# Optimization experiments

Measured on AMD Instinct MI355X. Metric: run time of the kernel, lower is better.

The kernel has to match this reference:

```python
import jax, jax.numpy as jnp
import numpy as np

B = 65536
N_FEATURES = 96
N_TOKENS = 32      # ceil(96/3)
DEPTH = 6
N_Q3_LAYERS = 6    # stem + 4 residual + 1 reduce (3to1)
N_CLASSES = 10


def setup_inputs() -> dict:
    key = jax.random.key(0)
    k1, k2, k3 = jax.random.split(key, 3)
    x_ = jax.random.normal(k1, (B, N_FEATURES), dtype=jnp.float32)
    # packed per-layer, per-block StronglyEntanglingLayers weights: (n_layers, n_tokens, depth, 3, 3)
    thetas = 0.01 * jax.random.normal(k2, (N_Q3_LAYERS, N_TOKENS, DEPTH, 3, 3), dtype=jnp.float32)
    w_cls = jax.random.normal(k3, (N_CLASSES, N_TOKENS), dtype=jnp.float32) / np.sqrt(N_TOKENS)
    b_cls = jnp.zeros((N_CLASSES,), dtype=jnp.float32)
    return {"x_": x_, "thetas": thetas, "w_cls": w_cls, "b_cls": b_cls}


def _rot(phi, theta, omega):
    """PennyLane Rot(phi,theta,omega) matrix, elementwise over leading dims -> (...,2,2) complex64."""
    ct = jnp.cos(0.5 * theta)
    st = jnp.sin(0.5 * theta)
    m00 = jnp.exp(-0.5j * (phi + omega)) * ct
    m01 = -jnp.exp(0.5j * (phi - omega)) * st
    m10 = jnp.exp(-0.5j * (phi - omega)) * st
    m11 = jnp.exp(0.5j * (phi + omega)) * ct
    return jnp.stack([jnp.stack([m00, m01], -1), jnp.stack([m10, m11], -1)], -2)


_EINS_1Q = ['kij,bkjmn->bkimn', 'kij,bkmjn->bkmin', 'kij,bkmnj->bkmni']


def _apply_1q(psi, U, w):
    # psi: (B,K,2,2,2); U: (K,2,2) one gate per block k
    return jnp.einsum(_EINS_1Q[w], U, psi)


def _apply_cnot(psi, c, t):
    cax = 2 + c
    p0 = jnp.take(psi, 0, axis=cax)
    p1 = jnp.take(psi, 1, axis=cax)
    tax = 2 + t - (1 if t > c else 0)  # target axis after removing control axis
    p1 = jnp.flip(p1, axis=tax)        # X on target where control=1
    return jnp.stack([p0, p1], axis=cax)


def _run_q3(x, W):
    """3-qubit circuits batched over (B, K) blocks.
    x: (B,K,3) angles; W: (K,depth,3,3) SEL weights. Returns <Z_0>,<Z_1>,<Z_2>: (B,K,3).
    AngleEmbedding(RY) on |000> gives a product state."""
    half = 0.5 * x
    amps = jnp.stack([jnp.cos(half), jnp.sin(half)], -1)  # (B,K,3,2)
    psi = jnp.einsum('bki,bkj,bkl->bkijl', amps[:, :, 0], amps[:, :, 1], amps[:, :, 2])
    psi = psi.astype(jnp.complex64)
    depth = W.shape[1]
    for l in range(depth):
        for w in range(3):
            U = _rot(W[:, l, w, 0], W[:, l, w, 1], W[:, l, w, 2])
            psi = _apply_1q(psi, U, w)
        r = (l % 2) + 1  # PennyLane default ranges for 3 wires: 1,2,1,2,...
        for w in range(3):
            psi = _apply_cnot(psi, w, (w + r) % 3)
    probs = psi.real ** 2 + psi.imag ** 2  # (B,K,2,2,2)
    zs = []
    for w in range(3):
        other = tuple(2 + i for i in range(3) if i != w)
        pm = probs.sum(axis=other)  # (B,K,2)
        zs.append(pm[..., 0] - pm[..., 1])
    return jnp.stack(zs, -1)


def reference(x_, thetas, w_cls, b_cls):
    Bsz = x_.shape[0]
    K = thetas.shape[1]
    padded = 3 * K
    tot = padded - x_.shape[1]
    pl = tot // 2
    H = jnp.pad(x_, ((0, 0), (pl, tot - pl)))  # (B, padded)
    # stem: mode='first' (contiguous blocks)
    H = _run_q3(H.reshape(Bsz, K, 3), thetas[0]).reshape(Bsz, padded)
    # residual layers: mode='fully' -> transpose block/position then re-chunk
    for l in range(1, thetas.shape[0] - 1):
        inp = H.reshape(Bsz, K, 3).transpose(0, 2, 1).reshape(Bsz, K, 3)
        H = _run_q3(inp, thetas[l]).reshape(Bsz, padded) + H
    # reduce: 3to1 per block -> <Z_0> only
    z = _run_q3(H.reshape(Bsz, K, 3), thetas[-1])[..., 0]  # (B, K)
    return z @ w_cls.T + b_cls
```

## Files before the change

kernel.cpp:

```cpp
#include <hip/hip_runtime.h>


#define INV2PI 0.15915494309189535f

typedef _Float16 hf2 __attribute__((ext_vector_type(2)));
typedef _Float16 hf4 __attribute__((ext_vector_type(4)));

#if __has_builtin(__builtin_amdgcn_fdot2)
#define HAVE_FDOT2 1
#else
#define HAVE_FDOT2 0
#endif

__device__ __forceinline__ float fdot2e(hf2 a, hf2 m, float acc) {
#if HAVE_FDOT2
  return __builtin_amdgcn_fdot2(a, m, acc, false);
#else
  return fmaf((float)a.x, (float)m.x, fmaf((float)a.y, (float)m.y, acc));
#endif
}

#if __has_builtin(__builtin_amdgcn_sinf)
__device__ __forceinline__ float hwsin(float r) { return __builtin_amdgcn_sinf(r); }
__device__ __forceinline__ float hwcos(float r) { return __builtin_amdgcn_cosf(r); }
#else
__device__ __forceinline__ float hwsin(float r) { return __sinf(r * 6.2831853071795865f); }
__device__ __forceinline__ float hwcos(float r) { return __cosf(r * 6.2831853071795865f); }
#endif

__global__ __launch_bounds__(256) void build_T(const float* __restrict__ thetas,
                                               hf2* __restrict__ Thp,
                                               hf2* __restrict__ T5) {
  __shared__ float Ur[32][8][8];
  __shared__ float Ui[32][8][8];
  const int l = blockIdx.x;
  const int t = threadIdx.x;
  const int k = t >> 3;
  const int col = t & 7;

  float pr[8], pi[8];
#pragma unroll
  for (int j = 0; j < 8; ++j) { pr[j] = (j == col) ? 1.f : 0.f; pi[j] = 0.f; }

  const float* th = thetas + (size_t)(l * 32 + k) * 54;
#pragma unroll
  for (int d = 0; d < 6; ++d) {
#pragma unroll
    for (int w = 0; w < 3; ++w) {
      float phi = th[(d * 3 + w) * 3 + 0];
      float tht = th[(d * 3 + w) * 3 + 1];
      float omg = th[(d * 3 + w) * 3 + 2];
      float st, ct, sp, cp, sm, cm;
      __sincosf(0.5f * tht, &st, &ct);
      __sincosf(0.5f * (phi + omg), &sp, &cp);
      __sincosf(0.5f * (phi - omg), &sm, &cm);
      float m00r =  cp * ct, m00i = -sp * ct;
      float m01r = -cm * st, m01i = -sm * st;
      float m10r =  cm * st, m10i = -sm * st;
      float m11r =  cp * ct, m11i =  sp * ct;
      const int s = 4 >> w;
#pragma unroll
      for (int base = 0; base < 8; ++base) {
        if (base & s) continue;
        float ar = pr[base], ai = pi[base];
        float br = pr[base + s], bi = pi[base + s];
        pr[base]     = m00r * ar - m00i * ai + m01r * br - m01i * bi;
        pi[base]     = m00r * ai + m00i * ar + m01r * bi + m01i * br;
        pr[base + s] = m10r * ar - m10i * ai + m11r * br - m11i * bi;
        pi[base + s] = m10r * ai + m10i * ar + m11r * bi + m11i * br;
      }
    }
    const int r = (d & 1) + 1;
#pragma unroll
    for (int w = 0; w < 3; ++w) {
      const int cs = 4 >> w;
      const int ts = 4 >> ((w + r) % 3);
#pragma unroll
      for (int idx = 0; idx < 8; ++idx) {
        if (!(idx & cs) || (idx & ts)) continue;
        const int j2 = idx | ts;
        float tr = pr[idx]; pr[idx] = pr[j2]; pr[j2] = tr;
        float ti = pi[idx]; pi[idx] = pi[j2]; pi[j2] = ti;
      }
    }
  }
#pragma unroll
  for (int j = 0; j < 8; ++j) { Ur[k][col][j] = pr[j]; Ui[k][col][j] = pi[j]; }
  __syncthreads();

  if (col < 3) {
    const int w = col;
    float rem[8][8];
#pragma unroll
    for (int a = 0; a < 8; ++a) {
#pragma unroll
      for (int bb = 0; bb < 8; ++bb) {
        float acc = 0.f;
#pragma unroll
        for (int c = 0; c < 8; ++c) {
          float zs = ((c >> (2 - w)) & 1) ? -1.f : 1.f;
          acc += zs * (Ur[k][a][c] * Ur[k][bb][c] + Ui[k][a][c] * Ui[k][bb][c]);
        }
        rem[a][bb] = acc;
      }
    }
    const int   ga[3][2] = {{0, 1}, {0, 1}, {0, 1}};
    const int   gb[3][2] = {{0, 1}, {0, 1}, {1, 0}};
    const float gc[3][2] = {{0.5f, 0.5f}, {0.5f, -0.5f}, {0.5f, 0.5f}};
    const int MONO[3][3] = {{0, 3, 4}, {1, 5, 6}, {2, 7, 8}};
    float tv[27];
#pragma unroll
    for (int p = 0; p < 3; ++p) {
#pragma unroll
      for (int q = 0; q < 3; ++q) {
#pragma unroll
        for (int rr = 0; rr < 3; ++rr) {
          float acc = 0.f;
#pragma unroll
          for (int e0 = 0; e0 < 2; ++e0)
#pragma unroll
            for (int e1 = 0; e1 < 2; ++e1)
#pragma unroll
              for (int e2 = 0; e2 < 2; ++e2) {
                int a  = (ga[p][e0] << 2) | (ga[q][e1] << 1) | ga[rr][e2];
                int bb = (gb[p][e0] << 2) | (gb[q][e1] << 1) | gb[rr][e2];
                acc += gc[p][e0] * gc[q][e1] * gc[rr][e2] * rem[a][bb];
              }
          tv[p * 9 + MONO[q][rr]] = acc;
        }
      }
    }
    if (l < 5) {
#pragma unroll
      for (int i = 0; i < 27; ++i) tv[i] *= INV2PI;
      hf2* Tp = Thp + ((size_t)(l * 32 + k)) * 48 + w * 16;
#pragma unroll
      for (int p = 0; p < 3; ++p) {
#pragma unroll
        for (int d = 0; d < 4; ++d) {
          hf2 v = {(_Float16)tv[p * 9 + 2 * d], (_Float16)tv[p * 9 + 2 * d + 1]};
          Tp[p * 5 + d] = v;
        }
        hf2 v4 = {(_Float16)tv[p * 9 + 8], (_Float16)0.f};
        Tp[p * 5 + 4] = v4;
      }
      hf2 zz = {(_Float16)0.f, (_Float16)0.f};
      Tp[15] = zz;
    } else if (w == 0) {
      hf2* Tp = T5 + k * 16;
#pragma unroll
      for (int p = 0; p < 3; ++p) {
#pragma unroll
        for (int d = 0; d < 4; ++d) {
          hf2 v = {(_Float16)tv[p * 9 + 2 * d], (_Float16)tv[p * 9 + 2 * d + 1]};
          Tp[p * 5 + d] = v;
        }
        hf2 v4 = {(_Float16)tv[p * 9 + 8], (_Float16)0.f};
        Tp[p * 5 + 4] = v4;
      }
      hf2 zz = {(_Float16)0.f, (_Float16)0.f};
      Tp[15] = zz;
    }
  }
}

__device__ __forceinline__ void evalk(const hf2* __restrict__ tb,
                                      float a0, float a1, float a2,
                                      float* __restrict__ z) {
  float s0 = hwsin(a0), c0 = hwcos(a0);
  float s1 = hwsin(a1), c1 = hwcos(a1);
  float s2 = hwsin(a2), c2 = hwcos(a2);
  float m5 = c1 * c2, m6 = c1 * s2, m7 = s1 * c2, m8 = s1 * s2;
  hf2 M0 = {(_Float16)1.0f, (_Float16)c1};
  hf2 M1 = {(_Float16)s1,   (_Float16)c2};
  hf2 M2 = {(_Float16)s2,   (_Float16)m5};
  hf2 M3 = {(_Float16)m6,   (_Float16)m7};
  hf2 M4 = {(_Float16)m8,   (_Float16)0.0f};
#pragma unroll
  for (int w = 0; w < 3; ++w) {
    const hf2* tw = tb + w * 16;
    float P[3];
#pragma unroll
    for (int p = 0; p < 3; ++p) {
      const hf2* tt = tw + p * 5;
      float acc = fdot2e(tt[0], M0, 0.0f);
      acc = fdot2e(tt[1], M1, acc);
      acc = fdot2e(tt[2], M2, acc);
      acc = fdot2e(tt[3], M3, acc);
      acc = fdot2e(tt[4], M4, acc);
      P[p] = acc;
    }
    z[w] = fmaf(s0, P[2], fmaf(c0, P[1], P[0]));
  }
}

__device__ __forceinline__ float evalk1(const hf2* __restrict__ tb,
                                        float a0, float a1, float a2) {
  float s0 = hwsin(a0), c0 = hwcos(a0);
  float s1 = hwsin(a1), c1 = hwcos(a1);
  float s2 = hwsin(a2), c2 = hwcos(a2);
  float m5 = c1 * c2, m6 = c1 * s2, m7 = s1 * c2, m8 = s1 * s2;
  hf2 M0 = {(_Float16)1.0f, (_Float16)c1};
  hf2 M1 = {(_Float16)s1,   (_Float16)c2};
  hf2 M2 = {(_Float16)s2,   (_Float16)m5};
  hf2 M3 = {(_Float16)m6,   (_Float16)m7};
  hf2 M4 = {(_Float16)m8,   (_Float16)0.0f};
  float P[3];
#pragma unroll
  for (int p = 0; p < 3; ++p) {
    const hf2* tt = tb + p * 5;
    float acc = fdot2e(tt[0], M0, 0.0f);
    acc = fdot2e(tt[1], M1, acc);
    acc = fdot2e(tt[2], M2, acc);
    acc = fdot2e(tt[3], M3, acc);
    acc = fdot2e(tt[4], M4, acc);
    P[p] = acc;
  }
  return fmaf(s0, P[2], fmaf(c0, P[1], P[0]));
}

__global__ __launch_bounds__(512, 8) void vqc_main(const float* __restrict__ x,
                                                   const hf2* __restrict__ Thp,
                                                   const hf2* __restrict__ T5,
                                                   const float* __restrict__ wcls,
                                                   const float* __restrict__ bcls,
                                                   float* __restrict__ out) {
  __shared__ __align__(16) _Float16 buf[2][64][96];
  const int t = threadIdx.x;
  const int b = t & 63;
  const int ws = __builtin_amdgcn_readfirstlane(t >> 6);
  const size_t b0 = (size_t)blockIdx.x * 64;

  const float4* xv = (const float4*)(x + b0 * 96);
#pragma unroll
  for (int i = 0; i < 3; ++i) {
    int f = t + i * 512;
    float4 v = xv[f];
    int d = 4 * f;
    int row = d / 96, col = d % 96;
    hf4 sv = {(_Float16)(v.x * INV2PI), (_Float16)(v.y * INV2PI),
              (_Float16)(v.z * INV2PI), (_Float16)(v.w * INV2PI)};
    *(hf4*)&buf[0][row][col] = sv;
  }
  __syncthreads();

  float h[4][3];

#pragma unroll
  for (int l = 0; l < 5; ++l) {
    const int cur = l & 1;
    float xin[12];
#pragma unroll
    for (int u = 0; u < 3; ++u) {
      hf4 v = *(const hf4*)&buf[cur][b][12 * ws + 4 * u];
      xin[4 * u + 0] = (float)v.x; xin[4 * u + 1] = (float)v.y;
      xin[4 * u + 2] = (float)v.z; xin[4 * u + 3] = (float)v.w;
    }
    const hf2* tb = Thp + ((size_t)l * 32 + 4 * ws) * 48;
    float z0[3], z1[3], z2[3], z3[3];
    evalk(tb + 0 * 48, xin[0], xin[1],  xin[2],  z0);
    evalk(tb + 1 * 48, xin[3], xin[4],  xin[5],  z1);
    evalk(tb + 2 * 48, xin[6], xin[7],  xin[8],  z2);
    evalk(tb + 3 * 48, xin[9], xin[10], xin[11], z3);
    if (l == 0) {
#pragma unroll
      for (int j = 0; j < 3; ++j) {
        h[0][j] = z0[j]; h[1][j] = z1[j]; h[2][j] = z2[j]; h[3][j] = z3[j];
      }
    } else {
#pragma unroll
      for (int j = 0; j < 3; ++j) {
        h[0][j] += z0[j]; h[1][j] += z1[j]; h[2][j] += z2[j]; h[3][j] += z3[j];
      }
    }
    if (l < 4) {
#pragma unroll
      for (int j = 0; j < 3; ++j) {
        hf4 wv = {(_Float16)h[0][j], (_Float16)h[1][j],
                  (_Float16)h[2][j], (_Float16)h[3][j]};
        *(hf4*)&buf[cur ^ 1][b][32 * j + 4 * ws] = wv;
      }
      __syncthreads();
    }
  }

  {
    float zs0 = evalk1(T5 + (4 * ws + 0) * 16, h[0][0], h[0][1], h[0][2]);
    float zs1 = evalk1(T5 + (4 * ws + 1) * 16, h[1][0], h[1][1], h[1][2]);
    float zs2 = evalk1(T5 + (4 * ws + 2) * 16, h[2][0], h[2][1], h[2][2]);
    float zs3 = evalk1(T5 + (4 * ws + 3) * 16, h[3][0], h[3][1], h[3][2]);
    hf4 zv = {(_Float16)zs0, (_Float16)zs1, (_Float16)zs2, (_Float16)zs3};
    *(hf4*)&buf[1][b][4 * ws] = zv;
  }
  __syncthreads();

  for (int idx = t; idx < 640; idx += 512) {
    int bb = idx / 10, c = idx % 10;
    float acc = bcls[c];
#pragma unroll
    for (int k = 0; k < 32; ++k)
      acc = fmaf((float)buf[1][bb][k], wcls[c * 32 + k], acc);
    out[(b0 + bb) * 10 + c] = acc;
  }
}

extern "C" void kernel_launch(void* const* d_in, const int* in_sizes, int n_in,
                              void* d_out, int out_size, void* d_ws, size_t ws_size,
                              hipStream_t stream) {
  const float* x  = (const float*)d_in[0];
  const float* th = (const float*)d_in[1];
  const float* wc = (const float*)d_in[2];
  const float* bc = (const float*)d_in[3];
  float* out = (float*)d_out;
  hf2* Thp = (hf2*)d_ws;
  hf2* T5  = Thp + 5 * 32 * 48;

  build_T<<<6, 256, 0, stream>>>(th, Thp, T5);
  vqc_main<<<65536 / 64, 512, 0, stream>>>(x, Thp, T5, wc, bc, out);
}
```

Measured before the change: 53.98 us.

## Stage per-layer circuit tables in double-buffered LDS with prefetch and vector loads

The per-layer polynomial coefficient tables used to be read from global memory with wave-uniform scalar loads. They are now copied cooperatively into a double-buffered shared-memory array, with the next layer's table prefetched into registers during the current layer. Within evalk the tables are read as 16-byte hf8 vectors. This replaces many scalar or global loads with a few LDS broadcast reads, at the cost of 12 KB more LDS per block (which may lower occupancy) and LDS reads in place of SGPR operands.

Result: slower. 68.09 us (+26.1%).

```diff
diff --git a/kernel.cpp b/kernel.cpp
--- a/kernel.cpp
+++ b/kernel.cpp
@@ -5,6 +5,7 @@
 
 typedef _Float16 hf2 __attribute__((ext_vector_type(2)));
 typedef _Float16 hf4 __attribute__((ext_vector_type(4)));
+typedef _Float16 hf8 __attribute__((ext_vector_type(8)));
 
 #if __has_builtin(__builtin_amdgcn_fdot2)
 #define HAVE_FDOT2 1
@@ -164,7 +165,7 @@
   }
 }
 
-__device__ __forceinline__ void evalk(const hf2* __restrict__ tb,
+__device__ __forceinline__ void evalk(const unsigned int* __restrict__ tkd,
                                       float a0, float a1, float a2,
                                       float* __restrict__ z) {
   float s0 = hwsin(a0), c0 = hwcos(a0);
@@ -178,19 +179,39 @@
   hf2 M4 = {(_Float16)m8,   (_Float16)0.0f};
 #pragma unroll
   for (int w = 0; w < 3; ++w) {
-    const hf2* tw = tb + w * 16;
-    float P[3];
-#pragma unroll
-    for (int p = 0; p < 3; ++p) {
-      const hf2* tt = tw + p * 5;
-      float acc = fdot2e(tt[0], M0, 0.0f);
-      acc = fdot2e(tt[1], M1, acc);
-      acc = fdot2e(tt[2], M2, acc);
-      acc = fdot2e(tt[3], M3, acc);
-      acc = fdot2e(tt[4], M4, acc);
-      P[p] = acc;
-    }
-    z[w] = fmaf(s0, P[2], fmaf(c0, P[1], P[0]));
+    const hf8* tv = (const hf8*)(tkd + w * 16);
+    hf8 A = tv[0], B = tv[1], C = tv[2], D = tv[3];
+    hf2 t00 = __builtin_shufflevector(A, A, 0, 1);
+    hf2 t01 = __builtin_shufflevector(A, A, 2, 3);
+    hf2 t02 = __builtin_shufflevector(A, A, 4, 5);
+    hf2 t03 = __builtin_shufflevector(A, A, 6, 7);
+    hf2 t04 = __builtin_shufflevector(B, B, 0, 1);
+    hf2 t10 = __builtin_shufflevector(B, B, 2, 3);
+    hf2 t11 = __builtin_shufflevector(B, B, 4, 5);
+    hf2 t12 = __builtin_shufflevector(B, B, 6, 7);
+    hf2 t13 = __builtin_shufflevector(C, C, 0, 1);
+    hf2 t14 = __builtin_shufflevector(C, C, 2, 3);
+    hf2 t20 = __builtin_shufflevector(C, C, 4, 5);
+    hf2 t21 = __builtin_shufflevector(C, C, 6, 7);
+    hf2 t22 = __builtin_shufflevector(D, D, 0, 1);
+    hf2 t23 = __builtin_shufflevector(D, D, 2, 3);
+    hf2 t24 = __builtin_shufflevector(D, D, 4, 5);
+    float P0 = fdot2e(t00, M0, 0.0f);
+    P0 = fdot2e(t01, M1, P0);
+    P0 = fdot2e(t02, M2, P0);
+    P0 = fdot2e(t03, M3, P0);
+    P0 = fdot2e(t04, M4, P0);
+    float P1 = fdot2e(t10, M0, 0.0f);
+    P1 = fdot2e(t11, M1, P1);
+    P1 = fdot2e(t12, M2, P1);
+    P1 = fdot2e(t13, M3, P1);
+    P1 = fdot2e(t14, M4, P1);
+    float P2 = fdot2e(t20, M0, 0.0f);
+    P2 = fdot2e(t21, M1, P2);
+    P2 = fdot2e(t22, M2, P2);
+    P2 = fdot2e(t23, M3, P2);
+    P2 = fdot2e(t24, M4, P2);
+    z[w] = fmaf(s0, P2, fmaf(c0, P1, P0));
   }
 }
 
@@ -226,11 +247,14 @@
                                                    const float* __restrict__ bcls,
                                                    float* __restrict__ out) {
   __shared__ __align__(16) _Float16 buf[2][64][96];
+  __shared__ __align__(16) unsigned int Tlds[2][1536];
   const int t = threadIdx.x;
   const int b = t & 63;
   const int ws = __builtin_amdgcn_readfirstlane(t >> 6);
   const size_t b0 = (size_t)blockIdx.x * 64;
-
+  const unsigned int* Tg = (const unsigned int*)Thp;
+
+  unsigned int p0 = Tg[t], p1 = Tg[t + 512], p2 = Tg[t + 1024];
   const float4* xv = (const float4*)(x + b0 * 96);
 #pragma unroll
   for (int i = 0; i < 3; ++i) {
@@ -242,6 +266,7 @@
               (_Float16)(v.z * INV2PI), (_Float16)(v.w * INV2PI)};
     *(hf4*)&buf[0][row][col] = sv;
   }
+  Tlds[0][t] = p0; Tlds[0][t + 512] = p1; Tlds[0][t + 1024] = p2;
   __syncthreads();
 
   float h[4][3];
@@ -249,6 +274,12 @@
 #pragma unroll
   for (int l = 0; l < 5; ++l) {
     const int cur = l & 1;
+    unsigned int q0 = 0, q1 = 0, q2 = 0;
+    if (l < 4) {
+      q0 = Tg[(l + 1) * 1536 + t];
+      q1 = Tg[(l + 1) * 1536 + t + 512];
+      q2 = Tg[(l + 1) * 1536 + t + 1024];
+    }
     float xin[12];
 #pragma unroll
     for (int u = 0; u < 3; ++u) {
@@ -256,7 +287,7 @@
       xin[4 * u + 0] = (float)v.x; xin[4 * u + 1] = (float)v.y;
       xin[4 * u + 2] = (float)v.z; xin[4 * u + 3] = (float)v.w;
     }
-    const hf2* tb = Thp + ((size_t)l * 32 + 4 * ws) * 48;
+    const unsigned int* tb = &Tlds[cur][(4 * ws) * 48];
     float z0[3], z1[3], z2[3], z3[3];
     evalk(tb + 0 * 48, xin[0], xin[1],  xin[2],  z0);
     evalk(tb + 1 * 48, xin[3], xin[4],  xin[5],  z1);
@@ -280,6 +311,7 @@
                   (_Float16)h[2][j], (_Float16)h[3][j]};
         *(hf4*)&buf[cur ^ 1][b][32 * j + 4 * ws] = wv;
       }
+      Tlds[cur ^ 1][t] = q0; Tlds[cur ^ 1][t + 512] = q1; Tlds[cur ^ 1][t + 1024] = q2;
       __syncthreads();
     }
   }
```

## Exchange packed sin/cos pairs via LDS and parallelize T-table build

Applied to the files above, without the earlier changes.

The producer of each activation now computes its sin/cos once and stores it as a packed fp16 pair in a single-buffered LDS exchange, with a barrier between read and write. Consumer threads no longer each evaluate sin/cos per layer, and the monomials are built with packed half multiplies. build_T is spread over 192 blocks of 64 threads so the per-block 8x8 reductions run in parallel, and fp16 conversions use round-toward-zero packing. The extra barrier per layer and RTZ rounding may cost some time and accuracy.

Result: faster. 46.43 us (-14.0%).

```diff
diff --git a/kernel.cpp b/kernel.cpp
--- a/kernel.cpp
+++ b/kernel.cpp
@@ -3,8 +3,8 @@
 
 #define INV2PI 0.15915494309189535f
 
+typedef unsigned int u32;
 typedef _Float16 hf2 __attribute__((ext_vector_type(2)));
-typedef _Float16 hf4 __attribute__((ext_vector_type(4)));
 
 #if __has_builtin(__builtin_amdgcn_fdot2)
 #define HAVE_FDOT2 1
@@ -28,154 +28,168 @@
 __device__ __forceinline__ float hwcos(float r) { return __cosf(r * 6.2831853071795865f); }
 #endif
 
-__global__ __launch_bounds__(256) void build_T(const float* __restrict__ thetas,
-                                               hf2* __restrict__ Thp,
-                                               hf2* __restrict__ T5) {
-  __shared__ float Ur[32][8][8];
-  __shared__ float Ui[32][8][8];
-  const int l = blockIdx.x;
+__device__ __forceinline__ hf2 pkrtz(float a, float b) {
+#if __has_builtin(__builtin_amdgcn_cvt_pkrtz)
+  return __builtin_bit_cast(hf2, __builtin_amdgcn_cvt_pkrtz(a, b));
+#else
+  hf2 v = {(_Float16)a, (_Float16)b};
+  return v;
+#endif
+}
+
+__device__ __forceinline__ u32 pk_sc(float hrev) {
+  return __builtin_bit_cast(u32, pkrtz(hwsin(hrev), hwcos(hrev)));
+}
+__device__ __forceinline__ hf2 as_hf2(u32 v) { return __builtin_bit_cast(hf2, v); }
+
+__global__ __launch_bounds__(64) void build_T(const float* __restrict__ thetas,
+                                              hf2* __restrict__ Thp,
+                                              hf2* __restrict__ T5) {
+  const int l = blockIdx.x >> 5;
+  const int k = blockIdx.x & 31;
   const int t = threadIdx.x;
-  const int k = t >> 3;
-  const int col = t & 7;
-
-  float pr[8], pi[8];
-#pragma unroll
-  for (int j = 0; j < 8; ++j) { pr[j] = (j == col) ? 1.f : 0.f; pi[j] = 0.f; }
-
-  const float* th = thetas + (size_t)(l * 32 + k) * 54;
-#pragma unroll
-  for (int d = 0; d < 6; ++d) {
+  __shared__ float Ur[8][8], Ui[8][8];
+  __shared__ float rem[3][8][8];
+  __shared__ float tvs[3][27];
+
+  if (t < 8) {
+    const int col = t;
+    float pr[8], pi[8];
+#pragma unroll
+    for (int j = 0; j < 8; ++j) { pr[j] = (j == col) ? 1.f : 0.f; pi[j] = 0.f; }
+    const float* th = thetas + (size_t)(l * 32 + k) * 54;
+#pragma unroll
+    for (int d = 0; d < 6; ++d) {
+#pragma unroll
+      for (int w = 0; w < 3; ++w) {
+        float phi = th[(d * 3 + w) * 3 + 0];
+        float tht = th[(d * 3 + w) * 3 + 1];
+        float omg = th[(d * 3 + w) * 3 + 2];
+        float st, ct, sp, cp, sm, cm;
+        __sincosf(0.5f * tht, &st, &ct);
+        __sincosf(0.5f * (phi + omg), &sp, &cp);
+        __sincosf(0.5f * (phi - omg), &sm, &cm);
+        float m00r =  cp * ct, m00i = -sp * ct;
+        float m01r = -cm * st, m01i = -sm * st;
+        float m10r =  cm * st, m10i = -sm * st;
+        float m11r =  cp * ct, m11i =  sp * ct;
+        const int s = 4 >> w;
+#pragma unroll
+        for (int base = 0; base < 8; ++base) {
+          if (base & s) continue;
+          float ar = pr[base], ai = pi[base];
+          float br = pr[base + s], bi = pi[base + s];
+          pr[base]     = m00r * ar - m00i * ai + m01r * br - m01i * bi;
+          pi[base]     = m00r * ai + m00i * ar + m01r * bi + m01i * br;
+          pr[base + s] = m10r * ar - m10i * ai + m11r * br - m11i * bi;
+          pi[base + s] = m10r * ai + m10i * ar + m11r * bi + m11i * br;
+        }
+      }
+      const int r = (d & 1) + 1;
+#pragma unroll
+      for (int w = 0; w < 3; ++w) {
+        const int cs = 4 >> w;
+        const int ts = 4 >> ((w + r) % 3);
+#pragma unroll
+        for (int idx = 0; idx < 8; ++idx) {
+          if (!(idx & cs) || (idx & ts)) continue;
+          const int j2 = idx | ts;
+          float tr = pr[idx]; pr[idx] = pr[j2]; pr[j2] = tr;
+          float ti = pi[idx]; pi[idx] = pi[j2]; pi[j2] = ti;
+        }
+      }
+    }
+#pragma unroll
+    for (int j = 0; j < 8; ++j) { Ur[col][j] = pr[j]; Ui[col][j] = pi[j]; }
+  }
+  __syncthreads();
+
+  {
+    const int a = t >> 3, bb = t & 7;
 #pragma unroll
     for (int w = 0; w < 3; ++w) {
-      float phi = th[(d * 3 + w) * 3 + 0];
-      float tht = th[(d * 3 + w) * 3 + 1];
-      float omg = th[(d * 3 + w) * 3 + 2];
-      float st, ct, sp, cp, sm, cm;
-      __sincosf(0.5f * tht, &st, &ct);
-      __sincosf(0.5f * (phi + omg), &sp, &cp);
-      __sincosf(0.5f * (phi - omg), &sm, &cm);
-      float m00r =  cp * ct, m00i = -sp * ct;
-      float m01r = -cm * st, m01i = -sm * st;
-      float m10r =  cm * st, m10i = -sm * st;
-      float m11r =  cp * ct, m11i =  sp * ct;
-      const int s = 4 >> w;
-#pragma unroll
-      for (int base = 0; base < 8; ++base) {
-        if (base & s) continue;
-        float ar = pr[base], ai = pi[base];
-        float br = pr[base + s], bi = pi[base + s];
-        pr[base]     = m00r * ar - m00i * ai + m01r * br - m01i * bi;
-        pi[base]     = m00r * ai + m00i * ar + m01r * bi + m01i * br;
-        pr[base + s] = m10r * ar - m10i * ai + m11r * br - m11i * bi;
-        pi[base + s] = m10r * ai + m10i * ar + m11r * bi + m11i * br;
-      }
-    }
-    const int r = (d & 1) + 1;
-#pragma unroll
-    for (int w = 0; w < 3; ++w) {
-      const int cs = 4 >> w;
-      const int ts = 4 >> ((w + r) % 3);
-#pragma unroll
-      for (int idx = 0; idx < 8; ++idx) {
-        if (!(idx & cs) || (idx & ts)) continue;
-        const int j2 = idx | ts;
-        float tr = pr[idx]; pr[idx] = pr[j2]; pr[j2] = tr;
-        float ti = pi[idx]; pi[idx] = pi[j2]; pi[j2] = ti;
-      }
-    }
-  }
-#pragma unroll
-  for (int j = 0; j < 8; ++j) { Ur[k][col][j] = pr[j]; Ui[k][col][j] = pi[j]; }
-  __syncthreads();
-
-  if (col < 3) {
-    const int w = col;
-    float rem[8][8];
-#pragma unroll
-    for (int a = 0; a < 8; ++a) {
-#pragma unroll
-      for (int bb = 0; bb < 8; ++bb) {
-        float acc = 0.f;
-#pragma unroll
-        for (int c = 0; c < 8; ++c) {
-          float zs = ((c >> (2 - w)) & 1) ? -1.f : 1.f;
-          acc += zs * (Ur[k][a][c] * Ur[k][bb][c] + Ui[k][a][c] * Ui[k][bb][c]);
-        }
-        rem[a][bb] = acc;
-      }
-    }
+      float acc = 0.f;
+#pragma unroll
+      for (int c = 0; c < 8; ++c) {
+        float zs = ((c >> (2 - w)) & 1) ? -1.f : 1.f;
+        acc += zs * (Ur[a][c] * Ur[bb][c] + Ui[a][c] * Ui[bb][c]);
+      }
+      rem[w][a][bb] = acc;
+    }
+  }
+  __syncthreads();
+
+  {
     const int   ga[3][2] = {{0, 1}, {0, 1}, {0, 1}};
     const int   gb[3][2] = {{0, 1}, {0, 1}, {1, 0}};
     const float gc[3][2] = {{0.5f, 0.5f}, {0.5f, -0.5f}, {0.5f, 0.5f}};
     const int MONO[3][3] = {{0, 3, 4}, {1, 5, 6}, {2, 7, 8}};
-    float tv[27];
-#pragma unroll
-    for (int p = 0; p < 3; ++p) {
-#pragma unroll
-      for (int q = 0; q < 3; ++q) {
-#pragma unroll
-        for (int rr = 0; rr < 3; ++rr) {
-          float acc = 0.f;
-#pragma unroll
-          for (int e0 = 0; e0 < 2; ++e0)
-#pragma unroll
-            for (int e1 = 0; e1 < 2; ++e1)
-#pragma unroll
-              for (int e2 = 0; e2 < 2; ++e2) {
-                int a  = (ga[p][e0] << 2) | (ga[q][e1] << 1) | ga[rr][e2];
-                int bb = (gb[p][e0] << 2) | (gb[q][e1] << 1) | gb[rr][e2];
-                acc += gc[p][e0] * gc[q][e1] * gc[rr][e2] * rem[a][bb];
-              }
-          tv[p * 9 + MONO[q][rr]] = acc;
-        }
-      }
-    }
-    if (l < 5) {
-#pragma unroll
-      for (int i = 0; i < 27; ++i) tv[i] *= INV2PI;
-      hf2* Tp = Thp + ((size_t)(l * 32 + k)) * 48 + w * 16;
-#pragma unroll
-      for (int p = 0; p < 3; ++p) {
-#pragma unroll
-        for (int d = 0; d < 4; ++d) {
-          hf2 v = {(_Float16)tv[p * 9 + 2 * d], (_Float16)tv[p * 9 + 2 * d + 1]};
-          Tp[p * 5 + d] = v;
-        }
-        hf2 v4 = {(_Float16)tv[p * 9 + 8], (_Float16)0.f};
-        Tp[p * 5 + 4] = v4;
-      }
-      hf2 zz = {(_Float16)0.f, (_Float16)0.f};
-      Tp[15] = zz;
-    } else if (w == 0) {
-      hf2* Tp = T5 + k * 16;
-#pragma unroll
-      for (int p = 0; p < 3; ++p) {
-#pragma unroll
-        for (int d = 0; d < 4; ++d) {
-          hf2 v = {(_Float16)tv[p * 9 + 2 * d], (_Float16)tv[p * 9 + 2 * d + 1]};
-          Tp[p * 5 + d] = v;
-        }
-        hf2 v4 = {(_Float16)tv[p * 9 + 8], (_Float16)0.f};
-        Tp[p * 5 + 4] = v4;
-      }
-      hf2 zz = {(_Float16)0.f, (_Float16)0.f};
-      Tp[15] = zz;
-    }
-  }
-}
-
-__device__ __forceinline__ void evalk(const hf2* __restrict__ tb,
-                                      float a0, float a1, float a2,
-                                      float* __restrict__ z) {
-  float s0 = hwsin(a0), c0 = hwcos(a0);
-  float s1 = hwsin(a1), c1 = hwcos(a1);
-  float s2 = hwsin(a2), c2 = hwcos(a2);
-  float m5 = c1 * c2, m6 = c1 * s2, m7 = s1 * c2, m8 = s1 * s2;
-  hf2 M0 = {(_Float16)1.0f, (_Float16)c1};
-  hf2 M1 = {(_Float16)s1,   (_Float16)c2};
-  hf2 M2 = {(_Float16)s2,   (_Float16)m5};
-  hf2 M3 = {(_Float16)m6,   (_Float16)m7};
-  hf2 M4 = {(_Float16)m8,   (_Float16)0.0f};
+    for (int e = t; e < 81; e += 64) {
+      int w = e / 27, re = e % 27;
+      int p = re / 9, q = (re % 9) / 3, r = re % 3;
+      float acc = 0.f;
+#pragma unroll
+      for (int e0 = 0; e0 < 2; ++e0)
+#pragma unroll
+        for (int e1 = 0; e1 < 2; ++e1)
+#pragma unroll
+          for (int e2 = 0; e2 < 2; ++e2) {
+            int a  = (ga[p][e0] << 2) | (ga[q][e1] << 1) | ga[r][e2];
+            int bb = (gb[p][e0] << 2) | (gb[q][e1] << 1) | gb[r][e2];
+            acc += gc[p][e0] * gc[q][e1] * gc[r][e2] * rem[w][a][bb];
+          }
+      tvs[w][p * 9 + MONO[q][r]] = acc;
+    }
+  }
+  __syncthreads();
+
+  if (l < 5) {
+    if (t < 48) {
+      int w = t >> 4, u = t & 15;
+      hf2 v;
+      if (u < 15) {
+        int p = u / 5, d = u % 5;
+        float lo = tvs[w][p * 9 + ((d == 4) ? 8 : 2 * d)] * INV2PI;
+        float hi = (d == 4) ? 0.f : tvs[w][p * 9 + 2 * d + 1] * INV2PI;
+        v = pkrtz(lo, hi);
+      } else {
+        v = pkrtz(0.f, 0.f);
+      }
+      Thp[((size_t)(l * 32 + k)) * 48 + w * 16 + u] = v;
+    }
+  } else {
+    if (t < 16) {
+      int u = t;
+      hf2 v;
+      if (u < 15) {
+        int p = u / 5, d = u % 5;
+        float lo = tvs[0][p * 9 + ((d == 4) ? 8 : 2 * d)];
+        float hi = (d == 4) ? 0.f : tvs[0][p * 9 + 2 * d + 1];
+        v = pkrtz(lo, hi);
+      } else {
+        v = pkrtz(0.f, 0.f);
+      }
+      T5[k * 16 + u] = v;
+    }
+  }
+}
+
+__device__ __forceinline__ void evalk_sc(const hf2* __restrict__ tb,
+                                         u32 cw, u32 aw, u32 bw,
+                                         float* __restrict__ z) {
+  hf2 C = as_hf2(cw), A = as_hf2(aw), B = as_hf2(bw);
+  hf2 Blo = __builtin_shufflevector(B, B, 0, 0);
+  hf2 Bhi = __builtin_shufflevector(B, B, 1, 1);
+  hf2 Pa = A * Blo;
+  hf2 Pb = A * Bhi;
+  const hf2 ONE2 = {(_Float16)1.0f, (_Float16)1.0f};
+  const hf2 ZERO2 = {(_Float16)0.0f, (_Float16)0.0f};
+  hf2 M0 = __builtin_shufflevector(ONE2, A, 0, 3);
+  hf2 M1 = __builtin_shufflevector(A, B, 0, 3);
+  hf2 M2 = __builtin_shufflevector(B, Pb, 0, 3);
+  hf2 M3 = __builtin_shufflevector(Pa, Pb, 1, 2);
+  hf2 M4 = __builtin_shufflevector(Pa, ZERO2, 0, 2);
+  float s0 = (float)C.x, c0 = (float)C.y;
 #pragma unroll
   for (int w = 0; w < 3; ++w) {
     const hf2* tw = tb + w * 16;
@@ -199,12 +213,11 @@
   float s0 = hwsin(a0), c0 = hwcos(a0);
   float s1 = hwsin(a1), c1 = hwcos(a1);
   float s2 = hwsin(a2), c2 = hwcos(a2);
-  float m5 = c1 * c2, m6 = c1 * s2, m7 = s1 * c2, m8 = s1 * s2;
-  hf2 M0 = {(_Float16)1.0f, (_Float16)c1};
-  hf2 M1 = {(_Float16)s1,   (_Float16)c2};
-  hf2 M2 = {(_Float16)s2,   (_Float16)m5};
-  hf2 M3 = {(_Float16)m6,   (_Float16)m7};
-  hf2 M4 = {(_Float16)m8,   (_Float16)0.0f};
+  hf2 M0 = pkrtz(1.0f, c1);
+  hf2 M1 = pkrtz(s1, c2);
+  hf2 M2 = pkrtz(s2, c1 * c2);
+  hf2 M3 = pkrtz(c1 * s2, s1 * c2);
+  hf2 M4 = pkrtz(s1 * s2, 0.f);
   float P[3];
 #pragma unroll
   for (int p = 0; p < 3; ++p) {
@@ -225,7 +238,7 @@
                                                    const float* __restrict__ wcls,
                                                    const float* __restrict__ bcls,
                                                    float* __restrict__ out) {
-  __shared__ __align__(16) _Float16 buf[2][64][96];
+  __shared__ u32 ex[64 * 100];
   const int t = threadIdx.x;
   const int b = t & 63;
   const int ws = __builtin_amdgcn_readfirstlane(t >> 6);
@@ -236,32 +249,31 @@
   for (int i = 0; i < 3; ++i) {
     int f = t + i * 512;
     float4 v = xv[f];
-    int d = 4 * f;
-    int row = d / 96, col = d % 96;
-    hf4 sv = {(_Float16)(v.x * INV2PI), (_Float16)(v.y * INV2PI),
-              (_Float16)(v.z * INV2PI), (_Float16)(v.w * INV2PI)};
-    *(hf4*)&buf[0][row][col] = sv;
+    int d = 4 * f, row = d / 96, col = d % 96;
+    uint4 pv;
+    pv.x = pk_sc(v.x * INV2PI);
+    pv.y = pk_sc(v.y * INV2PI);
+    pv.z = pk_sc(v.z * INV2PI);
+    pv.w = pk_sc(v.w * INV2PI);
+    *(uint4*)&ex[row * 100 + col] = pv;
   }
   __syncthreads();
 
   float h[4][3];
+  const int rb = b * 100 + 12 * ws;
 
 #pragma unroll
   for (int l = 0; l < 5; ++l) {
-    const int cur = l & 1;
-    float xin[12];
-#pragma unroll
-    for (int u = 0; u < 3; ++u) {
-      hf4 v = *(const hf4*)&buf[cur][b][12 * ws + 4 * u];
-      xin[4 * u + 0] = (float)v.x; xin[4 * u + 1] = (float)v.y;
-      xin[4 * u + 2] = (float)v.z; xin[4 * u + 3] = (float)v.w;
-    }
+    uint4 r0 = *(const uint4*)&ex[rb + 0];
+    uint4 r1 = *(const uint4*)&ex[rb + 4];
+    uint4 r2 = *(const uint4*)&ex[rb + 8];
+    __syncthreads();
     const hf2* tb = Thp + ((size_t)l * 32 + 4 * ws) * 48;
     float z0[3], z1[3], z2[3], z3[3];
-    evalk(tb + 0 * 48, xin[0], xin[1],  xin[2],  z0);
-    evalk(tb + 1 * 48, xin[3], xin[4],  xin[5],  z1);
-    evalk(tb + 2 * 48, xin[6], xin[7],  xin[8],  z2);
-    evalk(tb + 3 * 48, xin[9], xin[10], xin[11], z3);
+    evalk_sc(tb + 0 * 48, r0.x, r0.y, r0.z, z0);
+    evalk_sc(tb + 1 * 48, r0.w, r1.x, r1.y, z1);
+    evalk_sc(tb + 2 * 48, r1.z, r1.w, r2.x, z2);
+    evalk_sc(tb + 3 * 48, r2.y, r2.z, r2.w, z3);
     if (l == 0) {
 #pragma unroll
       for (int j = 0; j < 3; ++j) {
@@ -276,21 +288,24 @@
     if (l < 4) {
 #pragma unroll
       for (int j = 0; j < 3; ++j) {
-        hf4 wv = {(_Float16)h[0][j], (_Float16)h[1][j],
-                  (_Float16)h[2][j], (_Float16)h[3][j]};
-        *(hf4*)&buf[cur ^ 1][b][32 * j + 4 * ws] = wv;
+        uint4 wv;
+        wv.x = pk_sc(h[0][j]);
+        wv.y = pk_sc(h[1][j]);
+        wv.z = pk_sc(h[2][j]);
+        wv.w = pk_sc(h[3][j]);
+        *(uint4*)&ex[b * 100 + 32 * j + 4 * ws] = wv;
       }
       __syncthreads();
     }
   }
 
   {
-    float zs0 = evalk1(T5 + (4 * ws + 0) * 16, h[0][0], h[0][1], h[0][2]);
-    float zs1 = evalk1(T5 + (4 * ws + 1) * 16, h[1][0], h[1][1], h[1][2]);
-    float zs2 = evalk1(T5 + (4 * ws + 2) * 16, h[2][0], h[2][1], h[2][2]);
-    float zs3 = evalk1(T5 + (4 * ws + 3) * 16, h[3][0], h[3][1], h[3][2]);
-    hf4 zv = {(_Float16)zs0, (_Float16)zs1, (_Float16)zs2, (_Float16)zs3};
-    *(hf4*)&buf[1][b][4 * ws] = zv;
+    float4 zv;
+    zv.x = evalk1(T5 + (4 * ws + 0) * 16, h[0][0], h[0][1], h[0][2]);
+    zv.y = evalk1(T5 + (4 * ws + 1) * 16, h[1][0], h[1][1], h[1][2]);
+    zv.z = evalk1(T5 + (4 * ws + 2) * 16, h[2][0], h[2][1], h[2][2]);
+    zv.w = evalk1(T5 + (4 * ws + 3) * 16, h[3][0], h[3][1], h[3][2]);
+    *(float4*)&ex[b * 100 + 4 * ws] = zv;
   }
   __syncthreads();
 
@@ -299,7 +314,7 @@
     float acc = bcls[c];
 #pragma unroll
     for (int k = 0; k < 32; ++k)
-      acc = fmaf((float)buf[1][bb][k], wcls[c * 32 + k], acc);
+      acc = fmaf(__uint_as_float(ex[bb * 100 + k]), wcls[c * 32 + k], acc);
     out[(b0 + bb) * 10 + c] = acc;
   }
 }
@@ -315,6 +330,6 @@
   hf2* Thp = (hf2*)d_ws;
   hf2* T5  = Thp + 5 * 32 * 48;
 
-  build_T<<<6, 256, 0, stream>>>(th, Thp, T5);
+  build_T<<<192, 64, 0, stream>>>(th, Thp, T5);
   vqc_main<<<65536 / 64, 512, 0, stream>>>(x, Thp, T5, wc, bc, out);
 }
```
